# Kernel tuning notes

Measured on AMD Instinct MI355X. Metric: run time of the kernel, lower is better.

Reference implementation:

```python
import jax, jax.numpy as jnp
import numpy as np

B, T, D, H = 4, 2048, 1024, 16
HS = D // H

def _layernorm(x, g, b, eps=1e-5):
    mu = jnp.mean(x, axis=-1, keepdims=True)
    var = jnp.var(x, axis=-1, keepdims=True)
    return (x - mu) * jax.lax.rsqrt(var + eps) * g + b

def setup_inputs() -> dict:
    key = jax.random.key(0)
    ks = jax.random.split(key, 8)
    s = 0.02
    return {
        "x": jax.random.normal(ks[0], (B, T, D), jnp.float32),
        "wq": jax.random.normal(ks[1], (D, D), jnp.float32) * s,
        "wk": jax.random.normal(ks[2], (D, D), jnp.float32) * s,
        "wv": jax.random.normal(ks[3], (D, D), jnp.float32) * s,
        "wo": jax.random.normal(ks[4], (D, D), jnp.float32) * s,
        "bo": jnp.zeros((D,), jnp.float32),
        "w1": jax.random.normal(ks[5], (D, 4 * D), jnp.float32) * s,
        "b1": jnp.zeros((4 * D,), jnp.float32),
        "w2": jax.random.normal(ks[6], (4 * D, D), jnp.float32) * s,
        "b2": jnp.zeros((D,), jnp.float32),
        "g1": jnp.ones((D,), jnp.float32),
        "be1": jnp.zeros((D,), jnp.float32),
        "g2": jnp.ones((D,), jnp.float32),
        "be2": jnp.zeros((D,), jnp.float32),
    }

def reference(x, wq, wk, wv, wo, bo, w1, b1, w2, b2, g1, be1, g2, be2):
    b, t, d = x.shape
    h = H
    hs = d // h
    # --- pre-LN + multi-head causal self-attention ---
    xn = _layernorm(x, g1, be1)
    q = (xn @ wq).reshape(b, t, h, hs).transpose(0, 2, 1, 3)  # [b,h,t,hs]
    k = (xn @ wk).reshape(b, t, h, hs).transpose(0, 2, 1, 3)
    v = (xn @ wv).reshape(b, t, h, hs).transpose(0, 2, 1, 3)
    # NOTE: original scales by C**-0.5 where C = embedded_size (not head_size)
    scale = jnp.asarray(d, x.dtype) ** -0.5
    wei = jnp.einsum("bhqd,bhkd->bhqk", q, k) * scale
    causal = jnp.tril(jnp.ones((t, t), bool))
    wei = jnp.where(causal, wei, -jnp.inf)
    wei = jax.nn.softmax(wei, axis=-1)
    attn = jnp.einsum("bhqk,bhkd->bhqd", wei, v)
    attn = attn.transpose(0, 2, 1, 3).reshape(b, t, d)
    x = x + attn @ wo + bo
    # --- pre-LN + FFN ---
    xn2 = _layernorm(x, g2, be2)
    x = x + jax.nn.relu(xn2 @ w1 + b1) @ w2 + b2
    return x
```

## Files before the change

### kernel.cpp

```cpp
#include <hip/hip_runtime.h>
#include <hip/hip_bf16.h>
#include <stdint.h>

typedef __hip_bfloat16 bf16;
typedef __attribute__((ext_vector_type(8))) short bf16x8_t;
typedef __attribute__((ext_vector_type(4))) float f32x4_t;
typedef __attribute__((ext_vector_type(16))) float f32x16_t;
typedef __attribute__((ext_vector_type(2))) unsigned int u32x2_t;

#define B_ 4
#define T_ 2048
#define D_ 1024
#define H_ 16
#define HS_ 64
#define QKV_LD 3072

__device__ __forceinline__ void gload_lds16(const void* g, void* l) {
    __builtin_amdgcn_global_load_lds(
        (const __attribute__((address_space(1))) unsigned int*)g,
        (__attribute__((address_space(3))) unsigned int*)l, 16, 0, 0);
}

__device__ __forceinline__ bf16x8_t ldsv8(const bf16* p) {
    return *(const bf16x8_t*)p;
}

__device__ __forceinline__ unsigned pack2(float a, float b) {
    union { bf16 h[2]; unsigned u; } t;
    t.h[0] = __float2bfloat16(a);
    t.h[1] = __float2bfloat16(b);
    return t.u;
}

__global__ __launch_bounds__(256) void transpose_cvt(
    const float* __restrict__ W, bf16* __restrict__ WT, int K, int N)
{
    __shared__ float tile[32][33];
    const int nbx = N >> 5;
    const int bx = blockIdx.x % nbx;
    const int by = blockIdx.x / nbx;
    const int n0 = bx << 5, k0 = by << 5;
    const int tx = threadIdx.x & 31, ty = threadIdx.x >> 5;
#pragma unroll
    for (int i = 0; i < 32; i += 8)
        tile[ty + i][tx] = W[(long)(k0 + ty + i) * N + n0 + tx];
    __syncthreads();
#pragma unroll
    for (int i = 0; i < 32; i += 8)
        WT[(long)(n0 + ty + i) * K + k0 + tx] = __float2bfloat16(tile[tx][ty + i]);
}

__global__ __launch_bounds__(256) void vhead_transpose(
    const bf16* __restrict__ QKV, bf16* __restrict__ VT)
{
    __shared__ bf16 tile[32][33];
    int idx = blockIdx.x;
    const int tt  = idx & 63;   idx >>= 6;
    const int hst = idx & 1;    idx >>= 1;
    const int bh  = idx;
    const int b = bh >> 4, h = bh & 15;
    const int tx = threadIdx.x & 31, ty = threadIdx.x >> 5;
    const long vrow = (long)b * T_ + tt * 32;
    const int  vcol = 2048 + h * HS_ + hst * 32;
#pragma unroll
    for (int i = 0; i < 32; i += 8)
        tile[ty + i][tx] = QKV[(vrow + ty + i) * QKV_LD + vcol + tx];
    __syncthreads();
    const long orow = (long)bh * HS_ + hst * 32;
#pragma unroll
    for (int i = 0; i < 32; i += 8)
        VT[(orow + ty + i) * T_ + tt * 32 + tx] = tile[tx][ty + i];
}

__global__ __launch_bounds__(256) void ln_k(
    const float* __restrict__ x, const float* __restrict__ g,
    const float* __restrict__ be, bf16* __restrict__ out)
{
    const long row = blockIdx.x;
    const int t = threadIdx.x;
    const float4 v = ((const float4*)(x + row * D_))[t];
    float s  = v.x + v.y + v.z + v.w;
    float s2 = v.x * v.x + v.y * v.y + v.z * v.z + v.w * v.w;
#pragma unroll
    for (int m = 1; m < 64; m <<= 1) {
        s  += __shfl_xor(s, m, 64);
        s2 += __shfl_xor(s2, m, 64);
    }
    __shared__ float red[8];
    const int wv = t >> 6, ln = t & 63;
    if (ln == 0) { red[wv] = s; red[4 + wv] = s2; }
    __syncthreads();
    s  = red[0] + red[1] + red[2] + red[3];
    s2 = red[4] + red[5] + red[6] + red[7];
    const float mu  = s * (1.f / (float)D_);
    const float var = s2 * (1.f / (float)D_) - mu * mu;
    const float rs  = rsqrtf(var + 1e-5f);
    const float4 gv = ((const float4*)g)[t];
    const float4 bv = ((const float4*)be)[t];
    union { bf16 h[4]; short4 s4; } u;
    u.h[0] = __float2bfloat16((v.x - mu) * rs * gv.x + bv.x);
    u.h[1] = __float2bfloat16((v.y - mu) * rs * gv.y + bv.y);
    u.h[2] = __float2bfloat16((v.z - mu) * rs * gv.z + bv.z);
    u.h[3] = __float2bfloat16((v.w - mu) * rs * gv.w + bv.w);
    ((short4*)(out + row * D_))[t] = u.s4;
}

template<int HAS_BIAS, int RELU, int HAS_RES, int OUT_BF16>
__global__ __launch_bounds__(512, 1) void gemm2(
    const bf16* __restrict__ A, const bf16* __restrict__ BT,
    const float* __restrict__ bias, const float* __restrict__ res,
    void* __restrict__ Cout, int M, int N, int K)
{
    __shared__ bf16 As[2][256 * 64];
    __shared__ bf16 Bs[2][128 * 64];
    const int tid  = threadIdx.x;
    const int w    = tid >> 6;
    const int lane = tid & 63;
    const int wm = w >> 1, wn = w & 1;
    const int nbn = N >> 7;
    const int cpx = gridDim.x >> 3;
    const int bid = (blockIdx.x & 7) * cpx + (blockIdx.x >> 3);
    const int bm = bid / nbn, bn = bid % nbn;
    const int row0 = bm << 8, col0 = bn << 7;

    const bf16* aS0; const bf16* aS1; const bf16* aS2; const bf16* aS3;
    const bf16* bS0; const bf16* bS1;
    {
        int f0 = tid,        r0 = f0 >> 3, c0 = ((f0 & 7) ^ (r0 & 7)) << 3;
        int f1 = 512 + tid,  r1 = f1 >> 3, c1 = ((f1 & 7) ^ (r1 & 7)) << 3;
        int f2 = 1024 + tid, r2 = f2 >> 3, c2 = ((f2 & 7) ^ (r2 & 7)) << 3;
        int f3 = 1536 + tid, r3 = f3 >> 3, c3 = ((f3 & 7) ^ (r3 & 7)) << 3;
        aS0 = A + (long)(row0 + r0) * K + c0;
        aS1 = A + (long)(row0 + r1) * K + c1;
        aS2 = A + (long)(row0 + r2) * K + c2;
        aS3 = A + (long)(row0 + r3) * K + c3;
        bS0 = BT + (long)(col0 + r0) * K + c0;
        bS1 = BT + (long)(col0 + r1) * K + c1;
    }
    const int wbase = w * 64;

#define STAGE(buf, kt) do {                                              \
        const long ko_ = (long)(kt) * 64;                                \
        gload_lds16(aS0 + ko_, &As[buf][(0 * 512 + wbase) * 8]);         \
        gload_lds16(aS1 + ko_, &As[buf][(1 * 512 + wbase) * 8]);         \
        gload_lds16(aS2 + ko_, &As[buf][(2 * 512 + wbase) * 8]);         \
        gload_lds16(aS3 + ko_, &As[buf][(3 * 512 + wbase) * 8]);         \
        gload_lds16(bS0 + ko_, &Bs[buf][(0 * 512 + wbase) * 8]);         \
        gload_lds16(bS1 + ko_, &Bs[buf][(1 * 512 + wbase) * 8]);         \
    } while (0)

    f32x4_t acc[4][4] = {};
    const int fr = lane & 15;
    const int fq = lane >> 4;
    const int nt = K >> 6;

    STAGE(0, 0);
    STAGE(1, 1);

    for (int t = 0; t < nt; ++t) {
        const int cur = t & 1;
        if (t < nt - 1) asm volatile("s_waitcnt vmcnt(6)" ::: "memory");
        else            asm volatile("s_waitcnt vmcnt(0)" ::: "memory");
        __builtin_amdgcn_s_barrier();

        bf16x8_t a[2][4], b[2][4];
#pragma unroll
        for (int ks = 0; ks < 2; ++ks) {
#pragma unroll
            for (int m = 0; m < 4; ++m) {
                const int r = wm * 64 + m * 16 + fr;
                const int ch = ks * 4 + fq;
                a[ks][m] = ldsv8(&As[cur][r * 64 + ((ch ^ (r & 7)) << 3)]);
            }
#pragma unroll
            for (int n = 0; n < 4; ++n) {
                const int r = wn * 64 + n * 16 + fr;
                const int ch = ks * 4 + fq;
                b[ks][n] = ldsv8(&Bs[cur][r * 64 + ((ch ^ (r & 7)) << 3)]);
            }
        }
        asm volatile("s_waitcnt lgkmcnt(0)" ::: "memory");
        __builtin_amdgcn_sched_barrier(0);
        __builtin_amdgcn_s_barrier();

        if (t + 2 < nt) STAGE(cur, t + 2);

        __builtin_amdgcn_s_setprio(1);
#pragma unroll
        for (int m = 0; m < 4; ++m)
#pragma unroll
            for (int n = 0; n < 4; ++n) {
                acc[m][n] = __builtin_amdgcn_mfma_f32_16x16x32_bf16(a[0][m], b[0][n], acc[m][n], 0, 0, 0);
                acc[m][n] = __builtin_amdgcn_mfma_f32_16x16x32_bf16(a[1][m], b[1][n], acc[m][n], 0, 0, 0);
            }
        __builtin_amdgcn_s_setprio(0);
    }
#undef STAGE

    const int orow = fq << 2;
#pragma unroll
    for (int m = 0; m < 4; ++m) {
        const int rbase = row0 + wm * 64 + m * 16 + orow;
#pragma unroll
        for (int n = 0; n < 4; ++n) {
            const int c = col0 + wn * 64 + n * 16 + fr;
            float bv = 0.f;
            if (HAS_BIAS) bv = bias[c];
#pragma unroll
            for (int r = 0; r < 4; ++r) {
                float v = acc[m][n][r] + bv;
                if (RELU) v = fmaxf(v, 0.f);
                if (HAS_RES) v += res[(long)(rbase + r) * N + c];
                if (OUT_BF16)
                    ((bf16*)Cout)[(long)(rbase + r) * N + c] = __float2bfloat16(v);
                else
                    ((float*)Cout)[(long)(rbase + r) * N + c] = v;
            }
        }
    }
}

__device__ __forceinline__ void attn_tile(
    const bf16* K_, const bf16* V_, const bf16x8_t (&qf)[4],
    f32x16_t& oA, f32x16_t& oB, float& mOld, float& lSum,
    int c, int ct_w, int qabs, int w, int l31, int hi, int hi8, int swzk)
{
    const float kE  = 0.0450842200278f;
    const float THR = 256.0f;
    const bool diag = (c == ct_w);
    const bool two  = !(diag && !(w & 1));

    f32x16_t s0 = {}, s1 = {};
#pragma unroll
    for (int s = 0; s < 4; ++s) {
        bf16x8_t kf = ldsv8(K_ + l31 * 64 + ((16 * s + hi8) ^ swzk));
        s0 = __builtin_amdgcn_mfma_f32_32x32x16_bf16(kf, qf[s], s0, 0, 0, 0);
    }
    if (two) {
#pragma unroll
        for (int s = 0; s < 4; ++s) {
            bf16x8_t kf = ldsv8(K_ + (32 + l31) * 64 + ((16 * s + hi8) ^ swzk));
            s1 = __builtin_amdgcn_mfma_f32_32x32x16_bf16(kf, qf[s], s1, 0, 0, 0);
        }
    }

    if (diag) {
        const int stm = w & 1;
        const int kb0 = c * 64 + stm * 32 + 4 * hi;
        if (stm) {
#pragma unroll
            for (int r = 0; r < 16; ++r)
                if (kb0 + (r & 3) + 8 * (r >> 2) > qabs) s1[r] = -1e30f;
        } else {
#pragma unroll
            for (int r = 0; r < 16; ++r)
                if (kb0 + (r & 3) + 8 * (r >> 2) > qabs) s0[r] = -1e30f;
        }
    }

    float rm = s0[0];
#pragma unroll
    for (int r = 1; r < 16; ++r) rm = fmaxf(rm, s0[r]);
    if (two) {
#pragma unroll
        for (int r = 0; r < 16; ++r) rm = fmaxf(rm, s1[r]);
    }
    {
        u32x2_t rr = __builtin_amdgcn_permlane32_swap(
            __float_as_uint(rm), __float_as_uint(rm), false, false);
        rm = fmaxf(__uint_as_float(rr.x), __uint_as_float(rr.y));
    }
    if (!__all(rm <= mOld + THR)) {
        const float mN = fmaxf(mOld, rm);
        const float corr = exp2f((mOld - mN) * kE);
#pragma unroll
        for (int r = 0; r < 16; ++r) { oA[r] *= corr; oB[r] *= corr; }
        lSum *= corr;
        mOld = mN;
    }
    const float nmk = -mOld * kE;
#pragma unroll
    for (int r = 0; r < 16; ++r) s0[r] = exp2f(fmaf(s0[r], kE, nmk));
    if (two) {
#pragma unroll
        for (int r = 0; r < 16; ++r) s1[r] = exp2f(fmaf(s1[r], kE, nmk));
    }
    float rs = s0[0];
#pragma unroll
    for (int r = 1; r < 16; ++r) rs += s0[r];
    if (two) {
#pragma unroll
        for (int r = 0; r < 16; ++r) rs += s1[r];
    }
    {
        u32x2_t rr = __builtin_amdgcn_permlane32_swap(
            __float_as_uint(rs), __float_as_uint(rs), false, false);
        rs = __uint_as_float(rr.x) + __uint_as_float(rr.y);
    }
    lSum += rs;

    {
        unsigned pk_[8];
#pragma unroll
        for (int i = 0; i < 8; ++i) pk_[i] = pack2(s0[2 * i], s0[2 * i + 1]);
        union { unsigned u[4]; bf16x8_t v; } W0, W1;
        u32x2_t ra = __builtin_amdgcn_permlane32_swap(pk_[0], pk_[2], false, false);
        u32x2_t rb = __builtin_amdgcn_permlane32_swap(pk_[1], pk_[3], false, false);
        W0.u[0] = ra.x; W0.u[1] = rb.x; W0.u[2] = ra.y; W0.u[3] = rb.y;
        u32x2_t rc = __builtin_amdgcn_permlane32_swap(pk_[4], pk_[6], false, false);
        u32x2_t rd = __builtin_amdgcn_permlane32_swap(pk_[5], pk_[7], false, false);
        W1.u[0] = rc.x; W1.u[1] = rd.x; W1.u[2] = rc.y; W1.u[3] = rd.y;
#pragma unroll
        for (int m = 0; m < 2; ++m) {
            const int kcol = 16 * m + hi8;
            bf16x8_t vf0 = ldsv8(V_ + l31 * 64 + (kcol ^ swzk));
            oA = __builtin_amdgcn_mfma_f32_32x32x16_bf16(vf0, m ? W1.v : W0.v, oA, 0, 0, 0);
            bf16x8_t vf1 = ldsv8(V_ + (32 + l31) * 64 + (kcol ^ swzk));
            oB = __builtin_amdgcn_mfma_f32_32x32x16_bf16(vf1, m ? W1.v : W0.v, oB, 0, 0, 0);
        }
    }
    if (two) {
        unsigned pk_[8];
#pragma unroll
        for (int i = 0; i < 8; ++i) pk_[i] = pack2(s1[2 * i], s1[2 * i + 1]);
        union { unsigned u[4]; bf16x8_t v; } W0, W1;
        u32x2_t ra = __builtin_amdgcn_permlane32_swap(pk_[0], pk_[2], false, false);
        u32x2_t rb = __builtin_amdgcn_permlane32_swap(pk_[1], pk_[3], false, false);
        W0.u[0] = ra.x; W0.u[1] = rb.x; W0.u[2] = ra.y; W0.u[3] = rb.y;
        u32x2_t rc = __builtin_amdgcn_permlane32_swap(pk_[4], pk_[6], false, false);
        u32x2_t rd = __builtin_amdgcn_permlane32_swap(pk_[5], pk_[7], false, false);
        W1.u[0] = rc.x; W1.u[1] = rd.x; W1.u[2] = rc.y; W1.u[3] = rd.y;
#pragma unroll
        for (int m = 0; m < 2; ++m) {
            const int kcol = 16 * (2 + m) + hi8;
            bf16x8_t vf0 = ldsv8(V_ + l31 * 64 + (kcol ^ swzk));
            oA = __builtin_amdgcn_mfma_f32_32x32x16_bf16(vf0, m ? W1.v : W0.v, oA, 0, 0, 0);
            bf16x8_t vf1 = ldsv8(V_ + (32 + l31) * 64 + (kcol ^ swzk));
            oB = __builtin_amdgcn_mfma_f32_32x32x16_bf16(vf1, m ? W1.v : W0.v, oB, 0, 0, 0);
        }
    }
}

__global__ __launch_bounds__(512, 1) void attn_flash(
    const bf16* __restrict__ QKV, const bf16* __restrict__ VT,
    bf16* __restrict__ O)
{
    __shared__ bf16 Ks[2][64 * 64];
    __shared__ bf16 Vs[2][64 * 64];

    const int tid = threadIdx.x;
    const int w   = tid >> 6;
    const int ln  = tid & 63;
    const int l31 = ln & 31;
    const int hi  = ln >> 5;
    const int hi8 = hi << 3;

    const int qLo = blockIdx.x;
    const int qHi = 7 - qLo;
    const int bh = blockIdx.y;
    const long rowBase = (long)(bh >> 4) * T_;
    const int colBase = (bh & 15) * HS_;

    const int qabsL = qLo * 256 + w * 32 + l31;
    const int qabsH = qHi * 256 + w * 32 + l31;
    const int ct_L  = qLo * 4 + (w >> 1);
    const int ct_H  = qHi * 4 + (w >> 1);
    const int ctb   = qHi * 4 + 3;

    bf16x8_t qfL[4], qfH[4];
    {
        const bf16* qpL = QKV + (rowBase + qabsL) * QKV_LD + colBase + hi8;
        const bf16* qpH = QKV + (rowBase + qabsH) * QKV_LD + colBase + hi8;
#pragma unroll
        for (int s = 0; s < 4; ++s) {
            qfL[s] = *(const bf16x8_t*)(qpL + 16 * s);
            qfH[s] = *(const bf16x8_t*)(qpH + 16 * s);
        }
    }

    f32x16_t oLA = {}, oLB = {}, oHA = {}, oHB = {};
    float mL = -1e30f, lL = 0.f, mH = -1e30f, lH = 0.f;

    const int srow = tid >> 3;
    const int schunk = (((tid & 7) ^ (srow & 7)) << 3);
    const bf16* kSrc = QKV + (rowBase + srow) * QKV_LD + 1024 + colBase + schunk;
    const bf16* vSrc = VT + ((long)bh * HS_ + srow) * T_ + schunk;

    gload_lds16(kSrc, &Ks[0][w * 512]);
    gload_lds16(vSrc, &Vs[0][w * 512]);

    const int swzk = (l31 & 7) << 3;

    for (int c = 0; c <= ctb; ++c) {
        const int cur = c & 1;
        __syncthreads();

        if (c < ctb) {
            gload_lds16(kSrc + (long)(c + 1) * 64 * QKV_LD, &Ks[cur ^ 1][w * 512]);
            gload_lds16(vSrc + (c + 1) * 64, &Vs[cur ^ 1][w * 512]);
        }

        const bf16* K_ = Ks[cur];
        const bf16* V_ = Vs[cur];
        if (c <= ct_H)
            attn_tile(K_, V_, qfH, oHA, oHB, mH, lH, c, ct_H, qabsH, w, l31, hi, hi8, swzk);
        if (c <= ct_L)
            attn_tile(K_, V_, qfL, oLA, oLB, mL, lL, c, ct_L, qabsL, w, l31, hi, hi8, swzk);
    }

    {
        const float inv = 1.f / lH;
        bf16* Op = O + (rowBase + qabsH) * D_ + colBase;
#pragma unroll
        for (int g = 0; g < 4; ++g) {
            u32x2_t sA, sB;
            sA.x = pack2(oHA[4 * g + 0] * inv, oHA[4 * g + 1] * inv);
            sA.y = pack2(oHA[4 * g + 2] * inv, oHA[4 * g + 3] * inv);
            sB.x = pack2(oHB[4 * g + 0] * inv, oHB[4 * g + 1] * inv);
            sB.y = pack2(oHB[4 * g + 2] * inv, oHB[4 * g + 3] * inv);
            *(u32x2_t*)(Op + 8 * g + 4 * hi)      = sA;
            *(u32x2_t*)(Op + 32 + 8 * g + 4 * hi) = sB;
        }
    }
    {
        const float inv = 1.f / lL;
        bf16* Op = O + (rowBase + qabsL) * D_ + colBase;
#pragma unroll
        for (int g = 0; g < 4; ++g) {
            u32x2_t sA, sB;
            sA.x = pack2(oLA[4 * g + 0] * inv, oLA[4 * g + 1] * inv);
            sA.y = pack2(oLA[4 * g + 2] * inv, oLA[4 * g + 3] * inv);
            sB.x = pack2(oLB[4 * g + 0] * inv, oLB[4 * g + 1] * inv);
            sB.y = pack2(oLB[4 * g + 2] * inv, oLB[4 * g + 3] * inv);
            *(u32x2_t*)(Op + 8 * g + 4 * hi)      = sA;
            *(u32x2_t*)(Op + 32 + 8 * g + 4 * hi) = sB;
        }
    }
}

extern "C" void kernel_launch(void* const* d_in, const int* in_sizes, int n_in,
                              void* d_out, int out_size, void* d_ws, size_t ws_size,
                              hipStream_t stream)
{
    (void)in_sizes; (void)n_in; (void)out_size; (void)ws_size;
    const float* x   = (const float*)d_in[0];
    const float* wq  = (const float*)d_in[1];
    const float* wk  = (const float*)d_in[2];
    const float* wv  = (const float*)d_in[3];
    const float* wo  = (const float*)d_in[4];
    const float* bo  = (const float*)d_in[5];
    const float* w1  = (const float*)d_in[6];
    const float* b1  = (const float*)d_in[7];
    const float* w2  = (const float*)d_in[8];
    const float* b2  = (const float*)d_in[9];
    const float* g1  = (const float*)d_in[10];
    const float* be1 = (const float*)d_in[11];
    const float* g2  = (const float*)d_in[12];
    const float* be2 = (const float*)d_in[13];
    float* out = (float*)d_out;

    char* ws = (char*)d_ws;
    const size_t SLOT = (size_t)8192 * 1024 * 2;
    bf16* xn     = (bf16*)(ws);
    bf16* attnb  = (bf16*)(ws);
    bf16* qkv    = (bf16*)(ws + SLOT);
    bf16* xn2    = (bf16*)(ws + SLOT);
    bf16* vtb    = (bf16*)(ws + 4 * SLOT);
    bf16* hidden = (bf16*)(ws + 2 * SLOT);
    float* x1    = (float*)(ws + 6 * SLOT);
    char* wpos   = ws + 6 * SLOT + (size_t)33554432;
    bf16* wqkvT = (bf16*)(wpos);
    bf16* wqT = (bf16*)(wpos);
    bf16* wkT = (bf16*)(wpos + (size_t)2097152);
    bf16* wvT = (bf16*)(wpos + (size_t)2 * 2097152);
    bf16* woT = (bf16*)(wpos + (size_t)3 * 2097152);
    bf16* w1T = (bf16*)(wpos + (size_t)4 * 2097152);
    bf16* w2T = (bf16*)(wpos + (size_t)4 * 2097152 + 8388608);

    transpose_cvt<<<dim3(1024), 256, 0, stream>>>(wq, wqT, 1024, 1024);
    transpose_cvt<<<dim3(1024), 256, 0, stream>>>(wk, wkT, 1024, 1024);
    transpose_cvt<<<dim3(1024), 256, 0, stream>>>(wv, wvT, 1024, 1024);
    transpose_cvt<<<dim3(1024), 256, 0, stream>>>(wo, woT, 1024, 1024);
    transpose_cvt<<<dim3(4096), 256, 0, stream>>>(w1, w1T, 1024, 4096);
    transpose_cvt<<<dim3(4096), 256, 0, stream>>>(w2, w2T, 4096, 1024);

    ln_k<<<8192, 256, 0, stream>>>(x, g1, be1, xn);

    gemm2<0, 0, 0, 1><<<768, 512, 0, stream>>>(xn, wqkvT, nullptr, nullptr, qkv, 8192, 3072, 1024);

    vhead_transpose<<<8192, 256, 0, stream>>>(qkv, vtb);

    attn_flash<<<dim3(4, 64), 512, 0, stream>>>(qkv, vtb, attnb);

    gemm2<1, 0, 1, 0><<<256, 512, 0, stream>>>(attnb, woT, bo, x, x1, 8192, 1024, 1024);

    ln_k<<<8192, 256, 0, stream>>>(x1, g2, be2, xn2);

    gemm2<1, 1, 0, 1><<<1024, 512, 0, stream>>>(xn2, w1T, b1, nullptr, hidden, 8192, 4096, 1024);

    gemm2<1, 0, 1, 0><<<256, 512, 0, stream>>>(hidden, w2T, b2, x1, out, 8192, 1024, 4096);
}
```

Baseline: 504.3 us.

## Add 256x256-tile GEMM with phased K-split pipeline for QKV and FFN1

Adds a new gemm8 kernel with 256x256 output tiles (8x4 MFMA fragments per wave). The K-tile is split into two 32-wide halves that are staged and consumed in four interleaved phases, so loads for the next tile overlap with MFMA work, plus an XCD-aware block remap. It is used for the QKV projection and the first FFN GEMM to raise arithmetic intensity and cut LDS/global traffic per FLOP. In exchange it roughly doubles accumulator registers, adds more barriers, and halves the grid, which may leave CUs underfilled.

```diff
diff --git a/kernel.cpp b/kernel.cpp
--- a/kernel.cpp
+++ b/kernel.cpp
@@ -139,7 +139,7 @@
     }
     const int wbase = w * 64;
 
-#define STAGE(buf, kt) do {                                              \
+#define STAGE2(buf, kt) do {                                             \
         const long ko_ = (long)(kt) * 64;                                \
         gload_lds16(aS0 + ko_, &As[buf][(0 * 512 + wbase) * 8]);         \
         gload_lds16(aS1 + ko_, &As[buf][(1 * 512 + wbase) * 8]);         \
@@ -154,8 +154,8 @@
     const int fq = lane >> 4;
     const int nt = K >> 6;
 
-    STAGE(0, 0);
-    STAGE(1, 1);
+    STAGE2(0, 0);
+    STAGE2(1, 1);
 
     for (int t = 0; t < nt; ++t) {
         const int cur = t & 1;
@@ -183,7 +183,7 @@
         __builtin_amdgcn_sched_barrier(0);
         __builtin_amdgcn_s_barrier();
 
-        if (t + 2 < nt) STAGE(cur, t + 2);
+        if (t + 2 < nt) STAGE2(cur, t + 2);
 
         __builtin_amdgcn_s_setprio(1);
 #pragma unroll
@@ -195,12 +195,138 @@
             }
         __builtin_amdgcn_s_setprio(0);
     }
-#undef STAGE
+#undef STAGE2
 
     const int orow = fq << 2;
 #pragma unroll
     for (int m = 0; m < 4; ++m) {
         const int rbase = row0 + wm * 64 + m * 16 + orow;
+#pragma unroll
+        for (int n = 0; n < 4; ++n) {
+            const int c = col0 + wn * 64 + n * 16 + fr;
+            float bv = 0.f;
+            if (HAS_BIAS) bv = bias[c];
+#pragma unroll
+            for (int r = 0; r < 4; ++r) {
+                float v = acc[m][n][r] + bv;
+                if (RELU) v = fmaxf(v, 0.f);
+                if (HAS_RES) v += res[(long)(rbase + r) * N + c];
+                if (OUT_BF16)
+                    ((bf16*)Cout)[(long)(rbase + r) * N + c] = __float2bfloat16(v);
+                else
+                    ((float*)Cout)[(long)(rbase + r) * N + c] = v;
+            }
+        }
+    }
+}
+
+template<int HAS_BIAS, int RELU, int HAS_RES, int OUT_BF16>
+__global__ __launch_bounds__(512, 1) void gemm8(
+    const bf16* __restrict__ A, const bf16* __restrict__ BT,
+    const float* __restrict__ bias, const float* __restrict__ res,
+    void* __restrict__ Cout, int M, int N, int K)
+{
+    __shared__ bf16 As[2][2][256 * 32];
+    __shared__ bf16 Bs[2][2][256 * 32];
+
+    const int tid  = threadIdx.x;
+    const int w    = tid >> 6;
+    const int lane = tid & 63;
+    const int wm = w >> 2, wn = w & 3;
+    const int nbn = N >> 8;
+    const int cpx = gridDim.x >> 3;
+    const int bid = (blockIdx.x & 7) * cpx + (blockIdx.x >> 3);
+    const int bm = bid / nbn, bn = bid % nbn;
+    const int row0 = bm << 8, col0 = bn << 8;
+
+    const int r0s = tid >> 2;
+    const int c0s = (((tid & 3) ^ (r0s & 3)) << 3);
+    const bf16* aU0 = A  + (long)(row0 + r0s) * K + c0s;
+    const bf16* aU1 = aU0 + (long)128 * K;
+    const bf16* bU0 = BT + (long)(col0 + r0s) * K + c0s;
+    const bf16* bU1 = bU0 + (long)128 * K;
+    const int wb8 = w * 64 * 8;
+
+#define STAGE_A8(buf, kh, kt) do {                                        \
+        const long ko_ = (long)(kt) * 64 + (kh) * 32;                     \
+        gload_lds16(aU0 + ko_, &As[buf][kh][wb8]);                        \
+        gload_lds16(aU1 + ko_, &As[buf][kh][4096 + wb8]);                 \
+    } while (0)
+#define STAGE_B8(buf, kh, kt) do {                                        \
+        const long ko_ = (long)(kt) * 64 + (kh) * 32;                     \
+        gload_lds16(bU0 + ko_, &Bs[buf][kh][wb8]);                        \
+        gload_lds16(bU1 + ko_, &Bs[buf][kh][4096 + wb8]);                 \
+    } while (0)
+
+    f32x4_t acc[8][4] = {};
+    bf16x8_t af[8], bf0, bf1;
+    const int fr = lane & 15;
+    const int fq = lane >> 4;
+    const int nt = K >> 6;
+
+#define RD_A8(cur, ks) do { _Pragma("unroll")                              \
+        for (int m = 0; m < 8; ++m) {                                      \
+            const int rr = wm * 128 + m * 16 + fr;                         \
+            af[m] = ldsv8(&As[cur][ks][rr * 32 + ((fq ^ (rr & 3)) << 3)]); \
+        } } while (0)
+#define RD_B8(cur, ks, n) ldsv8(&Bs[cur][ks][(wn * 64 + (n) * 16 + fr) * 32 + \
+        ((fq ^ ((wn * 64 + (n) * 16 + fr) & 3)) << 3)])
+#define MM8(nh) do { _Pragma("unroll")                                     \
+        for (int m = 0; m < 8; ++m) {                                      \
+            acc[m][(nh)*2]   = __builtin_amdgcn_mfma_f32_16x16x32_bf16(af[m], bf0, acc[m][(nh)*2],   0, 0, 0); \
+            acc[m][(nh)*2+1] = __builtin_amdgcn_mfma_f32_16x16x32_bf16(af[m], bf1, acc[m][(nh)*2+1], 0, 0, 0); \
+        } } while (0)
+#define PHASE8(cur, ks, nh, RDA, STG, VM) do {                             \
+        if (RDA) RD_A8(cur, ks);                                           \
+        bf0 = RD_B8(cur, ks, (nh) * 2);                                    \
+        bf1 = RD_B8(cur, ks, (nh) * 2 + 1);                                \
+        STG;                                                               \
+        __builtin_amdgcn_s_barrier();                                      \
+        asm volatile("s_waitcnt lgkmcnt(0)" ::: "memory");                 \
+        __builtin_amdgcn_sched_barrier(0);                                 \
+        __builtin_amdgcn_s_setprio(1);                                     \
+        MM8(nh);                                                           \
+        __builtin_amdgcn_s_setprio(0);                                     \
+        VM;                                                                \
+        __builtin_amdgcn_s_barrier();                                      \
+    } while (0)
+#define VM4_ asm volatile("s_waitcnt vmcnt(4)" ::: "memory")
+#define VM0_ asm volatile("s_waitcnt vmcnt(0)" ::: "memory")
+
+    STAGE_A8(0, 0, 0);
+    STAGE_B8(0, 0, 0);
+    STAGE_A8(0, 1, 0);
+    STAGE_B8(0, 1, 0);
+    VM4_;
+    __builtin_amdgcn_s_barrier();
+
+    for (int t = 0; t < nt - 1; ++t) {
+        const int cur = t & 1, nb = cur ^ 1;
+        PHASE8(cur, 0, 0, 1, STAGE_A8(nb, 0, t + 1), (void)0);
+        PHASE8(cur, 0, 1, 0, STAGE_B8(nb, 0, t + 1), VM4_);
+        PHASE8(cur, 1, 0, 1, STAGE_A8(nb, 1, t + 1), (void)0);
+        PHASE8(cur, 1, 1, 0, STAGE_B8(nb, 1, t + 1), VM4_);
+    }
+    {
+        const int cur = (nt - 1) & 1;
+        PHASE8(cur, 0, 0, 1, (void)0, (void)0);
+        PHASE8(cur, 0, 1, 0, (void)0, VM0_);
+        PHASE8(cur, 1, 0, 1, (void)0, (void)0);
+        PHASE8(cur, 1, 1, 0, (void)0, (void)0);
+    }
+#undef STAGE_A8
+#undef STAGE_B8
+#undef RD_A8
+#undef RD_B8
+#undef MM8
+#undef PHASE8
+#undef VM4_
+#undef VM0_
+
+    const int orow = fq << 2;
+#pragma unroll
+    for (int m = 0; m < 8; ++m) {
+        const int rbase = row0 + wm * 128 + m * 16 + orow;
 #pragma unroll
         for (int n = 0; n < 4; ++n) {
             const int c = col0 + wn * 64 + n * 16 + fr;
@@ -486,7 +612,7 @@
 
     ln_k<<<8192, 256, 0, stream>>>(x, g1, be1, xn);
 
-    gemm2<0, 0, 0, 1><<<768, 512, 0, stream>>>(xn, wqkvT, nullptr, nullptr, qkv, 8192, 3072, 1024);
+    gemm8<0, 0, 0, 1><<<384, 512, 0, stream>>>(xn, wqkvT, nullptr, nullptr, qkv, 8192, 3072, 1024);
 
     vhead_transpose<<<8192, 256, 0, stream>>>(qkv, vtb);
 
@@ -496,7 +622,7 @@
 
     ln_k<<<8192, 256, 0, stream>>>(x1, g2, be2, xn2);
 
-    gemm2<1, 1, 0, 1><<<1024, 512, 0, stream>>>(xn2, w1T, b1, nullptr, hidden, 8192, 4096, 1024);
+    gemm8<1, 1, 0, 1><<<512, 512, 0, stream>>>(xn2, w1T, b1, nullptr, hidden, 8192, 4096, 1024);
 
     gemm2<1, 0, 1, 0><<<256, 512, 0, stream>>>(hidden, w2T, b2, x1, out, 8192, 1024, 4096);
 }
```

After: 505.5 us. No clear change (+0.2%).
